# Kernel tuning notes

Hardware: AMD Instinct MI355X
Metric: run time of the kernel (lower is better)

## Reference

```python
import jax, jax.numpy as jnp
import numpy as np

B, S, D = 4, 2048, 1024  # batch, seq_len, input_dimension
KD, VD = 1024, 1024      # key_dim, value_dim


def setup_inputs() -> dict:
    key = jax.random.key(0)
    ks = jax.random.split(key, 9)
    sc_in = 1.0 / np.sqrt(D)
    sc_v = 1.0 / np.sqrt(VD)
    return {
        "x":  jax.random.normal(ks[0], (B, S, D), dtype=jnp.float32),
        "Wq": jax.random.normal(ks[1], (KD, D), dtype=jnp.float32) * sc_in,
        "bq": jax.random.normal(ks[2], (KD,), dtype=jnp.float32) * 0.01,
        "Wk": jax.random.normal(ks[3], (KD, D), dtype=jnp.float32) * sc_in,
        "bk": jax.random.normal(ks[4], (KD,), dtype=jnp.float32) * 0.01,
        "Wv": jax.random.normal(ks[5], (VD, D), dtype=jnp.float32) * sc_in,
        "bv": jax.random.normal(ks[6], (VD,), dtype=jnp.float32) * 0.01,
        "Wo": jax.random.normal(ks[7], (D, VD), dtype=jnp.float32) * sc_v,
        "bo": jax.random.normal(ks[8], (D,), dtype=jnp.float32) * 0.01,
    }


def reference(x, Wq, bq, Wk, bk, Wv, bv, Wo, bo):
    # projections (torch Linear: x @ W.T + b)
    q = jnp.einsum('bsd,kd->bsk', x, Wq) + bq   # (B,S,KD)
    k = jnp.einsum('bsd,kd->bsk', x, Wk) + bk   # (B,S,KD)
    v = jnp.einsum('bsd,vd->bsv', x, Wv) + bv   # (B,S,VD)

    scores = jnp.einsum('bqk,bsk->bqs', q, k) / jnp.sqrt(jnp.float32(KD))  # (B,S,S)

    # sign rescale: scores * sign(scores) (sign(0) mapped to 1) == |scores| with zeros kept
    sign_mask = jnp.sign(scores)
    sign_mask = sign_mask + (sign_mask == 0).astype(jnp.float32)

    # causal mask: lower-triangular (incl diag) multiplied by 1, strict upper -> -inf
    seq = scores.shape[-1]
    causal = jnp.tril(jnp.ones((seq, seq), dtype=bool))
    masked = jnp.where(causal, scores * sign_mask, -jnp.inf)

    weights = jax.nn.softmax(masked, axis=2)            # (B,S,S)
    out = jnp.einsum('bqs,bsv->bqv', weights, v)        # (B,S,VD)
    return jnp.einsum('bqv,dv->bqd', out, Wo) + bo      # (B,S,D)
```

## Files before the change

kernel.cpp:

```cpp
#include <hip/hip_runtime.h>
#include <hip/hip_bf16.h>
#include <cstdint>


#define BM 128

typedef __attribute__((ext_vector_type(8))) __bf16 bf16x8;
typedef __attribute__((ext_vector_type(4))) __bf16 bf16x4;
typedef __attribute__((ext_vector_type(4))) float floatx4;

struct Ptr3 { const float* p[3]; };

__device__ __forceinline__ void async_copy16(const __bf16* g, const __bf16* l) {
  __builtin_amdgcn_global_load_lds(
      (const __attribute__((address_space(1))) unsigned int*)(const void*)g,
      (__attribute__((address_space(3))) unsigned int*)(unsigned)(uintptr_t)(const void*)l,
      16, 0, 0);
}

__device__ __forceinline__ void gemm_core(const __bf16* __restrict__ pA,
                                          const __bf16* __restrict__ pB,
                                          int K, int kBeg, int kEnd, int mb,
                                          int nb, floatx4 (&acc)[4][4]) {
  __shared__ __align__(16) __bf16 As0[BM * 32];
  __shared__ __align__(16) __bf16 As1[BM * 32];
  __shared__ __align__(16) __bf16 Bs0[BM * 32];
  __shared__ __align__(16) __bf16 Bs1[BM * 32];

  const int t = threadIdx.x;
  const int lane = t & 63;
  const int wave = t >> 6;
  const int quad = lane >> 4;
  const int l16 = lane & 15;
  const int wm = wave >> 1;
  const int wn = wave & 1;

  const __bf16* gA = pA + (long)(mb * BM + (t >> 2)) * K + ((t & 3) * 8);
  const __bf16* gB = pB + (long)(nb * BM + (t >> 2)) * K + ((t & 3) * 8);
  const long rowHalf = (long)64 * K;
  __bf16* lA0 = &As0[t * 8];
  __bf16* lA1 = &As1[t * 8];
  __bf16* lB0 = &Bs0[t * 8];
  __bf16* lB1 = &Bs1[t * 8];

  for (int kk = kBeg; kk < kEnd; ++kk) {
    const long ko = (long)kk * 64;
    async_copy16(gA + ko, lA0);
    async_copy16(gA + ko + rowHalf, lA0 + 2048);
    async_copy16(gA + ko + 32, lA1);
    async_copy16(gA + ko + 32 + rowHalf, lA1 + 2048);
    async_copy16(gB + ko, lB0);
    async_copy16(gB + ko + rowHalf, lB0 + 2048);
    async_copy16(gB + ko + 32, lB1);
    async_copy16(gB + ko + 32 + rowHalf, lB1 + 2048);
    __syncthreads();

#pragma unroll
    for (int p = 0; p < 2; ++p) {
      const __bf16* As = p ? As1 : As0;
      const __bf16* Bs = p ? Bs1 : Bs0;
      bf16x8 af[4], bfr[4];
#pragma unroll
      for (int i = 0; i < 4; ++i) {
        af[i] = *(const bf16x8*)&As[(wm * 64 + i * 16 + l16) * 32 + quad * 8];
        bfr[i] = *(const bf16x8*)&Bs[(wn * 64 + i * 16 + l16) * 32 + quad * 8];
      }
#pragma unroll
      for (int i = 0; i < 4; ++i)
#pragma unroll
        for (int j = 0; j < 4; ++j)
          acc[i][j] = __builtin_amdgcn_mfma_f32_16x16x32_bf16(af[i], bfr[j],
                                                              acc[i][j], 0, 0, 0);
    }
    __syncthreads();
  }
}

__global__ void __launch_bounds__(256, 3)
fusedA(const __bf16* __restrict__ xb, const __bf16* __restrict__ Wb,
       const float* __restrict__ bq, const float* __restrict__ bk,
       __bf16* __restrict__ qk, const __bf16* __restrict__ Wob,
       const __bf16* __restrict__ Wvt, __bf16* __restrict__ Wvo,
       int S, int KD, int B) {
  const int id = blockIdx.x;
  const __bf16 *pA, *pB;
  int mb, nb, z;
  if (id < 1024) {
    const int xcd = id & 7;
    const int j = id >> 3;
    mb = xcd * 8 + (j & 7);
    const int rest = j >> 3;
    nb = rest & 7;
    z = rest >> 3;
    pA = xb;
    pB = Wb + ((long)z << 20);
  } else {
    const int wid = id - 1024;
    mb = wid >> 3;
    nb = wid & 7;
    z = 2;
    pA = Wob;
    pB = Wvt;
  }

  floatx4 acc[4][4] = {};
  gemm_core(pA, pB, KD, 0, KD / 64, mb, nb, acc);

  const int t = threadIdx.x;
  const int lane = t & 63, wave = t >> 6;
  const int rb = (wave >> 1) * 64 + (lane >> 4) * 4;
  const int cb = (wave & 1) * 64 + (lane & 15);

  if (z < 2) {
    __bf16* C = qk + (long)z * B * S * KD;
    const float* bz = z ? bk : bq;
#pragma unroll
    for (int j4 = 0; j4 < 4; ++j4) {
      const int gc = nb * 128 + cb + j4 * 16;
      const float bv = bz[gc];
#pragma unroll
      for (int i = 0; i < 4; ++i) {
        const int gr = mb * BM + rb + i * 16;
#pragma unroll
        for (int r = 0; r < 4; ++r)
          C[(long)(gr + r) * KD + gc] = (__bf16)(acc[i][j4][r] + bv);
      }
    }
  } else {
#pragma unroll
    for (int j4 = 0; j4 < 4; ++j4) {
      const int gc = nb * 128 + cb + j4 * 16;
#pragma unroll
      for (int i = 0; i < 4; ++i) {
        const int gr = mb * BM + rb + i * 16;
#pragma unroll
        for (int r = 0; r < 4; ++r)
          Wvo[(long)(gr + r) * 1024 + gc] = (__bf16)acc[i][j4][r];
      }
    }
  }
}

__global__ void __launch_bounds__(256, 3)
fusedB(const __bf16* __restrict__ xb, const __bf16* __restrict__ Wvo,
       const float* __restrict__ bvo, __bf16* __restrict__ Ut,
       const __bf16* __restrict__ q, const __bf16* __restrict__ k,
       __bf16* __restrict__ P, float* __restrict__ lsum,
       int S, int KD, int D) {
  const int id = blockIdx.x;
  const __bf16 *pA, *pB;
  int mb, nb, b, mode;
  if (id < 512) {
    const int xcd = id & 7;
    const int j = id >> 3;
    mb = xcd * 8 + (j & 7);
    nb = j >> 3;
    b = 0;
    mode = 0;
    pA = xb;
    pB = Wvo;
  } else {
    const int sid = id - 512;
    const int xcd = sid & 7;
    const int r = sid >> 3;
    b = r / 17;
    const int ci = r - b * 17;
    const int n1 = xcd + 1;
    mb = (ci < n1) ? xcd : (15 - xcd);
    nb = (ci < n1) ? ci : (ci - n1);
    mode = 1;
    pA = q + (long)b * S * KD;
    pB = k + (long)b * S * KD;
  }

  floatx4 acc[4][4] = {};
  gemm_core(pA, pB, KD, 0, KD / 64, mb, nb, acc);

  const int t = threadIdx.x;
  const int lane = t & 63, wave = t >> 6;
  const int l16 = lane & 15;
  const int rb = (wave >> 1) * 64 + (lane >> 4) * 4;
  const int cb = (wave & 1) * 64 + l16;

  if (mode == 0) {
    const int bb = (mb * BM) / S;
    const int s0 = mb * BM - bb * S;
#pragma unroll
    for (int j4 = 0; j4 < 4; ++j4) {
      const int gc = nb * 128 + cb + j4 * 16;
      const float bv = bvo[gc];
#pragma unroll
      for (int i = 0; i < 4; ++i) {
        const int sr = s0 + rb + i * 16;
        bf16x4 o;
#pragma unroll
        for (int r = 0; r < 4; ++r) o[r] = (__bf16)(acc[i][j4][r] + bv);
        *(bf16x4*)&Ut[((long)bb * D + gc) * S + sr] = o;
      }
    }
  } else {
    __bf16* C = P + (long)b * S * S;
    float* lrow = lsum + (long)b * S;
    const float sc = 0.03125f;
#pragma unroll
    for (int i = 0; i < 4; ++i) {
#pragma unroll
      for (int r = 0; r < 4; ++r) {
        const int row = mb * BM + rb + i * 16 + r;
        float psum = 0.f;
#pragma unroll
        for (int j4 = 0; j4 < 4; ++j4) {
          const int col = nb * 128 + cb + j4 * 16;
          const float p = (col <= row) ? __expf(fabsf(acc[i][j4][r] * sc)) : 0.f;
          psum += p;
          C[(long)row * S + col] = (__bf16)p;
        }
        psum += __shfl_xor(psum, 1, 64);
        psum += __shfl_xor(psum, 2, 64);
        psum += __shfl_xor(psum, 4, 64);
        psum += __shfl_xor(psum, 8, 64);
        if (l16 == 0) atomicAdd(&lrow[row], psum);
      }
    }
  }
}

__global__ void __launch_bounds__(256, 3)
gemm_pvo(const __bf16* __restrict__ P, const __bf16* __restrict__ Ut,
         const float* __restrict__ lsum, const float* __restrict__ bo,
         float* __restrict__ out, int S, int D) {
  const int id = blockIdx.x;
  const int xcd = id & 7;
  const int j = id >> 3;
  const int half = j >> 5;
  const int idx = j & 31;
  const int b = idx >> 3;
  const int nb = idx & 7;
  const int mb = half ? xcd : (15 - xcd);

  floatx4 acc[4][4] = {};
  gemm_core(P + (long)b * S * S, Ut + (long)b * D * S, S, 0, 2 * (mb + 1), mb,
            nb, acc);

  const int t = threadIdx.x;
  const int lane = t & 63, wave = t >> 6;
  const int rb = (wave >> 1) * 64 + (lane >> 4) * 4;
  const int cb = (wave & 1) * 64 + (lane & 15);
  const float* lrow = lsum + (long)b * S;

#pragma unroll
  for (int i = 0; i < 4; ++i) {
#pragma unroll
    for (int r = 0; r < 4; ++r) {
      const int row = mb * BM + rb + i * 16 + r;
      const float inv = 1.f / lrow[row];
#pragma unroll
      for (int j4 = 0; j4 < 4; ++j4) {
        const int col = nb * 128 + cb + j4 * 16;
        out[((long)b * S + row) * D + col] = acc[i][j4][r] * inv + bo[col];
      }
    }
  }
}

__global__ void prep(const float* __restrict__ x, Ptr3 wp,
                     const float* __restrict__ Wv, const float* __restrict__ bv,
                     __bf16* __restrict__ xb, __bf16* __restrict__ Wb,
                     __bf16* __restrict__ Wvt, float* __restrict__ bvo,
                     float* __restrict__ lsum) {
  __shared__ __bf16 tile[64][66];
  __shared__ float wsum[4];
  const int bid = blockIdx.x;
  const int t = threadIdx.x;
  if (bid < 8192) {
    const long i = ((long)bid * 256 + t) * 4;
    const float4 f = *(const float4*)(x + i);
    bf16x4 o;
    o[0] = (__bf16)f.x; o[1] = (__bf16)f.y; o[2] = (__bf16)f.z; o[3] = (__bf16)f.w;
    *(bf16x4*)(xb + i) = o;
  } else if (bid < 11264) {
    const int slot = (bid - 8192) * 256 + t;
    const int which = slot >> 18;
    const long e = (long)(slot & 0x3ffff) * 4;
    const float4 f = *(const float4*)(wp.p[which] + e);
    bf16x4 o;
    o[0] = (__bf16)f.x; o[1] = (__bf16)f.y; o[2] = (__bf16)f.z; o[3] = (__bf16)f.w;
    *(bf16x4*)(Wb + ((long)which << 20) + e) = o;
  } else if (bid < 11520) {
    const int idx = bid - 11264;
    const int r0 = (idx >> 4) * 64, c0 = (idx & 15) * 64;
#pragma unroll
    for (int e = 0; e < 16; ++e) {
      const int i = e * 256 + t;
      const int r = i >> 6, c = i & 63;
      tile[r][c] = (__bf16)Wv[(long)(r0 + r) * 1024 + (c0 + c)];
    }
    __syncthreads();
#pragma unroll
    for (int e = 0; e < 16; ++e) {
      const int i = e * 256 + t;
      const int r = i >> 6, c = i & 63;
      Wvt[(long)(c0 + r) * 1024 + (r0 + c)] = tile[c][r];
    }
  } else if (bid < 12544) {
    const int d = bid - 11520;
    const float* row = wp.p[2] + (long)d * 1024;
    float s = 0.f;
    for (int v = t; v < 1024; v += 256) s += bv[v] * row[v];
#pragma unroll
    for (int off = 32; off > 0; off >>= 1) s += __shfl_down(s, off, 64);
    if ((t & 63) == 0) wsum[t >> 6] = s;
    __syncthreads();
    if (t == 0) bvo[d] = wsum[0] + wsum[1] + wsum[2] + wsum[3];
  } else {
#pragma unroll
    for (int e = 0; e < 8; ++e)
      *(float4*)(lsum + (e * 256 + t) * 4) = float4{0.f, 0.f, 0.f, 0.f};
  }
}

extern "C" void kernel_launch(void* const* d_in, const int* in_sizes, int n_in,
                              void* d_out, int out_size, void* d_ws, size_t ws_size,
                              hipStream_t stream) {
  const float* x = (const float*)d_in[0];
  const float* Wq = (const float*)d_in[1];
  const float* bq = (const float*)d_in[2];
  const float* Wk = (const float*)d_in[3];
  const float* bk = (const float*)d_in[4];
  const float* Wv = (const float*)d_in[5];
  const float* bv = (const float*)d_in[6];
  const float* Wo = (const float*)d_in[7];
  const float* bo = (const float*)d_in[8];
  float* out = (float*)d_out;

  constexpr int B = 4, S = 2048, D = 1024, KD = 1024;
  constexpr long MB_ = 1024 * 1024;

  char* w = (char*)d_ws;
  __bf16* xb = (__bf16*)(w);
  __bf16* qk = (__bf16*)(w + 16 * MB_);
  __bf16* Ut = (__bf16*)(w + 48 * MB_);
  __bf16* P  = (__bf16*)(w + 64 * MB_);
  __bf16* Wb = (__bf16*)(w + 96 * MB_);
  __bf16* Wvt = (__bf16*)(w + 102 * MB_);
  __bf16* Wvo = (__bf16*)(w + 104 * MB_);
  float* lsum = (float*)(w + 106 * MB_);
  float* bvo = (float*)(w + 106 * MB_ + 65536);

  __bf16* Wob = Wb + (2l << 20);

  Ptr3 wp{{Wq, Wk, Wo}};
  prep<<<12545, 256, 0, stream>>>(x, wp, Wv, bv, xb, Wb, Wvt, bvo, lsum);

  fusedA<<<1088, 256, 0, stream>>>(xb, Wb, bq, bk, qk, Wob, Wvt, Wvo, S, KD, B);

  fusedB<<<1056, 256, 0, stream>>>(xb, Wvo, bvo, Ut, qk, qk + (long)B * S * KD,
                                   P, lsum, S, KD, D);

  gemm_pvo<<<512, 256, 0, stream>>>(P, Ut, lsum, bo, out, S, D);
}
```

Before: 245.4 us.

## Fold Q/K projections into a precomputed Wq^T·Wk matrix with bias vectors

Scores are rewritten as x·(Wq^T Wk)·x^T plus rank-one bias terms. The kernel precomputes M = Wq^T Wk (a small 1024^3 GEMM), a column-bias vector and a per-row scalar correction u, then forms one projected tensor y2 = x·M + m2 and computes scores as y2·x^T + u. This replaces the two full-size Q and K projection GEMMs with one, which should cut a large share of the total matrix-multiply work. The fp32-to-bf16 conversion of x moves into the first GEMM launch, and preprocessing becomes a separate transpose kernel. In exchange there is an extra kernel launch, and rounding the combined matrix to bf16 may shift numerical error.

```diff
diff --git a/kernel.cpp b/kernel.cpp
--- a/kernel.cpp
+++ b/kernel.cpp
@@ -76,75 +76,206 @@
   }
 }
 
+__global__ void prep2(const float* __restrict__ Wo, Ptr3 tp,
+                      const float* __restrict__ bv, const float* __restrict__ bq,
+                      const float* __restrict__ bk,
+                      __bf16* __restrict__ Wob, __bf16* __restrict__ Wqt,
+                      __bf16* __restrict__ Wkt, __bf16* __restrict__ Wvt,
+                      float* __restrict__ bvo, float* __restrict__ cscal,
+                      float* __restrict__ lsum) {
+  __shared__ __bf16 tile[64][66];
+  __shared__ float wsum[4];
+  const int bid = blockIdx.x;
+  const int t = threadIdx.x;
+  if (bid < 1024) {
+    const long e = ((long)bid * 256 + t) * 4;
+    const float4 f = *(const float4*)(Wo + e);
+    bf16x4 o;
+    o[0] = (__bf16)f.x; o[1] = (__bf16)f.y; o[2] = (__bf16)f.z; o[3] = (__bf16)f.w;
+    *(bf16x4*)(Wob + e) = o;
+  } else if (bid < 1792) {
+    const int seg = (bid - 1024) >> 8;
+    const int idx = (bid - 1024) & 255;
+    const float* src = tp.p[seg];
+    __bf16* dstw = seg == 0 ? Wqt : (seg == 1 ? Wkt : Wvt);
+    const int r0 = (idx >> 4) * 64, c0 = (idx & 15) * 64;
+#pragma unroll
+    for (int e = 0; e < 16; ++e) {
+      const int i = e * 256 + t;
+      const int r = i >> 6, c = i & 63;
+      tile[r][c] = (__bf16)src[(long)(r0 + r) * 1024 + (c0 + c)];
+    }
+    __syncthreads();
+#pragma unroll
+    for (int e = 0; e < 16; ++e) {
+      const int i = e * 256 + t;
+      const int r = i >> 6, c = i & 63;
+      dstw[(long)(c0 + r) * 1024 + (r0 + c)] = tile[c][r];
+    }
+  } else if (bid < 2816) {
+    const int d = bid - 1792;
+    const float* row = Wo + (long)d * 1024;
+    float s = 0.f;
+    for (int v = t; v < 1024; v += 256) s += bv[v] * row[v];
+#pragma unroll
+    for (int off = 32; off > 0; off >>= 1) s += __shfl_down(s, off, 64);
+    if ((t & 63) == 0) wsum[t >> 6] = s;
+    __syncthreads();
+    if (t == 0) bvo[d] = wsum[0] + wsum[1] + wsum[2] + wsum[3];
+  } else if (bid == 2816) {
+    float s = 0.f;
+    for (int i = t; i < 1024; i += 256) s += bq[i] * bk[i];
+#pragma unroll
+    for (int off = 32; off > 0; off >>= 1) s += __shfl_down(s, off, 64);
+    if ((t & 63) == 0) wsum[t >> 6] = s;
+    __syncthreads();
+    if (t == 0) *cscal = wsum[0] + wsum[1] + wsum[2] + wsum[3];
+  } else {
+#pragma unroll
+    for (int e = 0; e < 8; ++e)
+      *(float4*)(lsum + (e * 256 + t) * 4) = float4{0.f, 0.f, 0.f, 0.f};
+  }
+}
+
 __global__ void __launch_bounds__(256, 3)
-fusedA(const __bf16* __restrict__ xb, const __bf16* __restrict__ Wb,
-       const float* __restrict__ bq, const float* __restrict__ bk,
-       __bf16* __restrict__ qk, const __bf16* __restrict__ Wob,
-       const __bf16* __restrict__ Wvt, __bf16* __restrict__ Wvo,
-       int S, int KD, int B) {
+gemmA(const __bf16* __restrict__ Wkt, const __bf16* __restrict__ Wqt,
+      const __bf16* __restrict__ Wob, const __bf16* __restrict__ Wvt,
+      __bf16* __restrict__ Mt, __bf16* __restrict__ Wvo,
+      const float* __restrict__ bk, const float* __restrict__ bq,
+      float* __restrict__ m1f, float* __restrict__ m2f,
+      const float* __restrict__ x, __bf16* __restrict__ xb) {
   const int id = blockIdx.x;
+  const int t = threadIdx.x;
+
+  if (id >= 160) {
+    const long i = ((long)(id - 160) * 256 + t) * 4;
+    const float4 f = *(const float4*)(x + i);
+    bf16x4 o;
+    o[0] = (__bf16)f.x; o[1] = (__bf16)f.y; o[2] = (__bf16)f.z; o[3] = (__bf16)f.w;
+    *(bf16x4*)(xb + i) = o;
+    return;
+  }
+  if (id >= 128) {
+    const int q = (id - 128) & 15;
+    const bool isM2 = (id - 128) >= 16;
+    const __bf16* Wt = isM2 ? Wkt : Wqt;
+    const float* bvec = isM2 ? bq : bk;
+    float* dst = isM2 ? m2f : m1f;
+    const int lane = t & 63, wave = t >> 6, qd = lane >> 4, l16 = lane & 15;
+#pragma unroll
+    for (int rr = 0; rr < 4; ++rr) {
+      const int row = q * 64 + (wave * 4 + qd) * 4 + rr;
+      const __bf16* wr = Wt + (long)row * 1024 + l16 * 64;
+      const float* bp = bvec + l16 * 64;
+      float s = 0.f;
+#pragma unroll
+      for (int jj = 0; jj < 8; ++jj) {
+        bf16x8 wv = *(const bf16x8*)(wr + jj * 8);
+#pragma unroll
+        for (int e = 0; e < 8; ++e) s += (float)wv[e] * bp[jj * 8 + e];
+      }
+      s += __shfl_xor(s, 1, 64);
+      s += __shfl_xor(s, 2, 64);
+      s += __shfl_xor(s, 4, 64);
+      s += __shfl_xor(s, 8, 64);
+      if (l16 == 0) dst[row] = s;
+    }
+    return;
+  }
+
   const __bf16 *pA, *pB;
-  int mb, nb, z;
-  if (id < 1024) {
-    const int xcd = id & 7;
-    const int j = id >> 3;
-    mb = xcd * 8 + (j & 7);
-    const int rest = j >> 3;
-    nb = rest & 7;
-    z = rest >> 3;
-    pA = xb;
-    pB = Wb + ((long)z << 20);
+  __bf16* dst;
+  int mb, nb;
+  if (id < 64) {
+    mb = id >> 3; nb = id & 7;
+    pA = Wkt; pB = Wqt; dst = Mt;
   } else {
-    const int wid = id - 1024;
-    mb = wid >> 3;
-    nb = wid & 7;
-    z = 2;
-    pA = Wob;
-    pB = Wvt;
+    const int w = id - 64;
+    mb = w >> 3; nb = w & 7;
+    pA = Wob; pB = Wvt; dst = Wvo;
   }
 
   floatx4 acc[4][4] = {};
-  gemm_core(pA, pB, KD, 0, KD / 64, mb, nb, acc);
-
-  const int t = threadIdx.x;
+  gemm_core(pA, pB, 1024, 0, 16, mb, nb, acc);
+
   const int lane = t & 63, wave = t >> 6;
   const int rb = (wave >> 1) * 64 + (lane >> 4) * 4;
   const int cb = (wave & 1) * 64 + (lane & 15);
-
-  if (z < 2) {
-    __bf16* C = qk + (long)z * B * S * KD;
-    const float* bz = z ? bk : bq;
-#pragma unroll
-    for (int j4 = 0; j4 < 4; ++j4) {
-      const int gc = nb * 128 + cb + j4 * 16;
-      const float bv = bz[gc];
-#pragma unroll
-      for (int i = 0; i < 4; ++i) {
-        const int gr = mb * BM + rb + i * 16;
-#pragma unroll
-        for (int r = 0; r < 4; ++r)
-          C[(long)(gr + r) * KD + gc] = (__bf16)(acc[i][j4][r] + bv);
-      }
-    }
-  } else {
-#pragma unroll
-    for (int j4 = 0; j4 < 4; ++j4) {
-      const int gc = nb * 128 + cb + j4 * 16;
-#pragma unroll
-      for (int i = 0; i < 4; ++i) {
-        const int gr = mb * BM + rb + i * 16;
-#pragma unroll
-        for (int r = 0; r < 4; ++r)
-          Wvo[(long)(gr + r) * 1024 + gc] = (__bf16)acc[i][j4][r];
-      }
+#pragma unroll
+  for (int j4 = 0; j4 < 4; ++j4) {
+    const int gc = nb * 128 + cb + j4 * 16;
+#pragma unroll
+    for (int i = 0; i < 4; ++i) {
+      const int gr = mb * BM + rb + i * 16;
+#pragma unroll
+      for (int r = 0; r < 4; ++r)
+        dst[(long)(gr + r) * 1024 + gc] = (__bf16)acc[i][j4][r];
     }
   }
 }
 
 __global__ void __launch_bounds__(256, 3)
-fusedB(const __bf16* __restrict__ xb, const __bf16* __restrict__ Wvo,
+gemmB1(const __bf16* __restrict__ xb, const __bf16* __restrict__ Mt,
+       const float* __restrict__ m2f, __bf16* __restrict__ y2,
+       const float* __restrict__ m1f, const float* __restrict__ cscal,
+       float* __restrict__ uvec) {
+  const int id = blockIdx.x;
+  const int t = threadIdx.x;
+
+  if (id >= 512) {
+    const int k = id - 512;
+    const int lane = t & 63, wave = t >> 6, qd = lane >> 4, l16 = lane & 15;
+    const float c = *cscal;
+#pragma unroll
+    for (int rr = 0; rr < 4; ++rr) {
+      const int row = k * 64 + (wave * 4 + qd) * 4 + rr;
+      const __bf16* xr = xb + (long)row * 1024 + l16 * 64;
+      const float* mp = m1f + l16 * 64;
+      float s = 0.f;
+#pragma unroll
+      for (int jj = 0; jj < 8; ++jj) {
+        bf16x8 xv = *(const bf16x8*)(xr + jj * 8);
+#pragma unroll
+        for (int e = 0; e < 8; ++e) s += (float)xv[e] * mp[jj * 8 + e];
+      }
+      s += __shfl_xor(s, 1, 64);
+      s += __shfl_xor(s, 2, 64);
+      s += __shfl_xor(s, 4, 64);
+      s += __shfl_xor(s, 8, 64);
+      if (l16 == 0) uvec[row] = s + c;
+    }
+    return;
+  }
+
+  const int xcd = id & 7;
+  const int j = id >> 3;
+  const int mb = xcd * 8 + (j & 7);
+  const int nb = j >> 3;
+
+  floatx4 acc[4][4] = {};
+  gemm_core(xb, Mt, 1024, 0, 16, mb, nb, acc);
+
+  const int lane = t & 63, wave = t >> 6;
+  const int rb = (wave >> 1) * 64 + (lane >> 4) * 4;
+  const int cb = (wave & 1) * 64 + (lane & 15);
+#pragma unroll
+  for (int j4 = 0; j4 < 4; ++j4) {
+    const int gc = nb * 128 + cb + j4 * 16;
+    const float bvv = m2f[gc];
+#pragma unroll
+    for (int i = 0; i < 4; ++i) {
+      const int gr = mb * BM + rb + i * 16;
+#pragma unroll
+      for (int r = 0; r < 4; ++r)
+        y2[(long)(gr + r) * 1024 + gc] = (__bf16)(acc[i][j4][r] + bvv);
+    }
+  }
+}
+
+__global__ void __launch_bounds__(256, 3)
+gemmB2(const __bf16* __restrict__ xb, const __bf16* __restrict__ Wvo,
        const float* __restrict__ bvo, __bf16* __restrict__ Ut,
-       const __bf16* __restrict__ q, const __bf16* __restrict__ k,
+       const __bf16* __restrict__ y2, const float* __restrict__ uvec,
        __bf16* __restrict__ P, float* __restrict__ lsum,
        int S, int KD, int D) {
   const int id = blockIdx.x;
@@ -169,8 +300,8 @@
     mb = (ci < n1) ? xcd : (15 - xcd);
     nb = (ci < n1) ? ci : (ci - n1);
     mode = 1;
-    pA = q + (long)b * S * KD;
-    pB = k + (long)b * S * KD;
+    pA = y2 + (long)b * S * KD;
+    pB = xb + (long)b * S * KD;
   }
 
   floatx4 acc[4][4] = {};
@@ -207,11 +338,13 @@
 #pragma unroll
       for (int r = 0; r < 4; ++r) {
         const int row = mb * BM + rb + i * 16 + r;
+        const float urow = uvec[(long)b * S + row];
         float psum = 0.f;
 #pragma unroll
         for (int j4 = 0; j4 < 4; ++j4) {
           const int col = nb * 128 + cb + j4 * 16;
-          const float p = (col <= row) ? __expf(fabsf(acc[i][j4][r] * sc)) : 0.f;
+          const float p =
+              (col <= row) ? __expf(fabsf(acc[i][j4][r] + urow) * sc) : 0.f;
           psum += p;
           C[(long)row * S + col] = (__bf16)p;
         }
@@ -260,62 +393,6 @@
         out[((long)b * S + row) * D + col] = acc[i][j4][r] * inv + bo[col];
       }
     }
-  }
-}
-
-__global__ void prep(const float* __restrict__ x, Ptr3 wp,
-                     const float* __restrict__ Wv, const float* __restrict__ bv,
-                     __bf16* __restrict__ xb, __bf16* __restrict__ Wb,
-                     __bf16* __restrict__ Wvt, float* __restrict__ bvo,
-                     float* __restrict__ lsum) {
-  __shared__ __bf16 tile[64][66];
-  __shared__ float wsum[4];
-  const int bid = blockIdx.x;
-  const int t = threadIdx.x;
-  if (bid < 8192) {
-    const long i = ((long)bid * 256 + t) * 4;
-    const float4 f = *(const float4*)(x + i);
-    bf16x4 o;
-    o[0] = (__bf16)f.x; o[1] = (__bf16)f.y; o[2] = (__bf16)f.z; o[3] = (__bf16)f.w;
-    *(bf16x4*)(xb + i) = o;
-  } else if (bid < 11264) {
-    const int slot = (bid - 8192) * 256 + t;
-    const int which = slot >> 18;
-    const long e = (long)(slot & 0x3ffff) * 4;
-    const float4 f = *(const float4*)(wp.p[which] + e);
-    bf16x4 o;
-    o[0] = (__bf16)f.x; o[1] = (__bf16)f.y; o[2] = (__bf16)f.z; o[3] = (__bf16)f.w;
-    *(bf16x4*)(Wb + ((long)which << 20) + e) = o;
-  } else if (bid < 11520) {
-    const int idx = bid - 11264;
-    const int r0 = (idx >> 4) * 64, c0 = (idx & 15) * 64;
-#pragma unroll
-    for (int e = 0; e < 16; ++e) {
-      const int i = e * 256 + t;
-      const int r = i >> 6, c = i & 63;
-      tile[r][c] = (__bf16)Wv[(long)(r0 + r) * 1024 + (c0 + c)];
-    }
-    __syncthreads();
-#pragma unroll
-    for (int e = 0; e < 16; ++e) {
-      const int i = e * 256 + t;
-      const int r = i >> 6, c = i & 63;
-      Wvt[(long)(c0 + r) * 1024 + (r0 + c)] = tile[c][r];
-    }
-  } else if (bid < 12544) {
-    const int d = bid - 11520;
-    const float* row = wp.p[2] + (long)d * 1024;
-    float s = 0.f;
-    for (int v = t; v < 1024; v += 256) s += bv[v] * row[v];
-#pragma unroll
-    for (int off = 32; off > 0; off >>= 1) s += __shfl_down(s, off, 64);
-    if ((t & 63) == 0) wsum[t >> 6] = s;
-    __syncthreads();
-    if (t == 0) bvo[d] = wsum[0] + wsum[1] + wsum[2] + wsum[3];
-  } else {
-#pragma unroll
-    for (int e = 0; e < 8; ++e)
-      *(float4*)(lsum + (e * 256 + t) * 4) = float4{0.f, 0.f, 0.f, 0.f};
   }
 }
 
@@ -337,25 +414,33 @@
   constexpr long MB_ = 1024 * 1024;
 
   char* w = (char*)d_ws;
-  __bf16* xb = (__bf16*)(w);
-  __bf16* qk = (__bf16*)(w + 16 * MB_);
-  __bf16* Ut = (__bf16*)(w + 48 * MB_);
-  __bf16* P  = (__bf16*)(w + 64 * MB_);
-  __bf16* Wb = (__bf16*)(w + 96 * MB_);
-  __bf16* Wvt = (__bf16*)(w + 102 * MB_);
-  __bf16* Wvo = (__bf16*)(w + 104 * MB_);
-  float* lsum = (float*)(w + 106 * MB_);
-  float* bvo = (float*)(w + 106 * MB_ + 65536);
-
-  __bf16* Wob = Wb + (2l << 20);
-
-  Ptr3 wp{{Wq, Wk, Wo}};
-  prep<<<12545, 256, 0, stream>>>(x, wp, Wv, bv, xb, Wb, Wvt, bvo, lsum);
-
-  fusedA<<<1088, 256, 0, stream>>>(xb, Wb, bq, bk, qk, Wob, Wvt, Wvo, S, KD, B);
-
-  fusedB<<<1056, 256, 0, stream>>>(xb, Wvo, bvo, Ut, qk, qk + (long)B * S * KD,
-                                   P, lsum, S, KD, D);
+  __bf16* xb  = (__bf16*)(w);
+  __bf16* y2  = (__bf16*)(w + 16 * MB_);
+  __bf16* Ut  = (__bf16*)(w + 32 * MB_);
+  __bf16* P   = (__bf16*)(w + 48 * MB_);
+  __bf16* Wob = (__bf16*)(w + 80 * MB_);
+  __bf16* Wqt = (__bf16*)(w + 82 * MB_);
+  __bf16* Wkt = (__bf16*)(w + 84 * MB_);
+  __bf16* Wvt = (__bf16*)(w + 86 * MB_);
+  __bf16* Mt  = (__bf16*)(w + 88 * MB_);
+  __bf16* Wvo = (__bf16*)(w + 90 * MB_);
+  float* lsum  = (float*)(w + 92 * MB_);
+  float* uvec  = (float*)(w + 92 * MB_ + 32768);
+  float* bvo   = (float*)(w + 92 * MB_ + 65536);
+  float* m2f   = (float*)(w + 92 * MB_ + 69632);
+  float* m1f   = (float*)(w + 92 * MB_ + 73728);
+  float* cscal = (float*)(w + 92 * MB_ + 77824);
+
+  Ptr3 tp{{Wq, Wk, Wv}};
+  prep2<<<2818, 256, 0, stream>>>(Wo, tp, bv, bq, bk, Wob, Wqt, Wkt, Wvt,
+                                  bvo, cscal, lsum);
+
+  gemmA<<<8352, 256, 0, stream>>>(Wkt, Wqt, Wob, Wvt, Mt, Wvo, bk, bq,
+                                  m1f, m2f, x, xb);
+
+  gemmB1<<<640, 256, 0, stream>>>(xb, Mt, m2f, y2, m1f, cscal, uvec);
+
+  gemmB2<<<1056, 256, 0, stream>>>(xb, Wvo, bvo, Ut, y2, uvec, P, lsum, S, KD, D);
 
   gemm_pvo<<<512, 256, 0, stream>>>(P, Ut, lsum, bo, out, S, D);
 }
```

Measured after the change: 243.0 us. No clear change (-1.0%).
